# Optimization experiments

Hardware: AMD Instinct MI355X
Metric: run time of the kernel (lower is better)

Reference implementation:

```python
import jax, jax.numpy as jnp
import numpy as np

FACTOR = 5  # sampling factor c

def setup_inputs() -> dict:
    key = jax.random.key(0)
    k1, k2, k3, k4 = jax.random.split(key, 4)
    B, H, L, D = 4, 8, 2048, 64
    u = min(max(1, FACTOR * int(np.ceil(np.log(L)))), L)  # sample_k = 40
    return {
        "queries": jax.random.normal(k1, (B, H, L, D), jnp.float32),
        "keys": jax.random.normal(k2, (B, H, L, D), jnp.float32),
        "values": jax.random.normal(k3, (B, H, L, D), jnp.float32),
        "index_sample": jax.random.randint(k4, (L, u), 0, L, jnp.int32),
    }

def reference(queries, keys, values, index_sample):
    B, H, L_Q, D = queries.shape
    L_K = keys.shape[2]
    scale = 1.0 / np.sqrt(D)
    U_part = min(max(1, FACTOR * int(np.ceil(np.log(L_K)))), L_Q)  # n_top queries

    # --- _prob_QK: sampled scores + sparsity measure ---
    # K_sample[b,h,q,s,:] = keys[b,h,index_sample[q,s],:]  -> (B,H,L_Q,u,D)
    K_sample = keys[:, :, index_sample, :]
    QK_sample = jnp.einsum('bhqd,bhqsd->bhqs', queries, K_sample)  # (B,H,L_Q,u)
    M = QK_sample.max(-1) - QK_sample.sum(-1) / L_K                # (B,H,L_Q)
    _, index = jax.lax.top_k(M, U_part)                            # (B,H,U)

    # --- initial context: mean of V for non-selected queries ---
    context = jnp.broadcast_to(values.mean(-2, keepdims=True), (B, H, L_Q, D))

    # --- full attention for the top-U queries only ---
    Q_reduce = jnp.take_along_axis(queries, index[..., None], axis=2)   # (B,H,U,D)
    scores = jnp.einsum('bhud,bhkd->bhuk', Q_reduce, keys) * scale      # (B,H,U,L_K)
    attn = jax.nn.softmax(scores, axis=-1)
    out = jnp.einsum('bhuk,bhkd->bhud', attn, values)                   # (B,H,U,D)

    # --- scatter selected outputs back into the mean context ---
    bi = jnp.arange(B)[:, None, None]
    hi = jnp.arange(H)[None, :, None]
    context = context.at[bi, hi, index].set(out)
    return context
```

## Files before the change

### kernel.cpp

```cpp
#include <hip/hip_runtime.h>
#include <math.h>

#define Bq 4
#define Hh 8
#define Lh 2048
#define Dh 64
#define BH (Bq*Hh)

__global__ __launch_bounds__(256) void kAC(const float* __restrict__ Q,
                                           const float* __restrict__ K,
                                           const float* __restrict__ V,
                                           const int* __restrict__ idxs,
                                           float2* __restrict__ M2,
                                           float* __restrict__ vpart, int u) {
    int bi = blockIdx.x;
    int tid = threadIdx.x;
    if (bi >= 256) {
        int b2 = bi - 256;
        int xcd = b2 & 7, slot = b2 >> 3;
        int bh  = xcd * 4 + (slot >> 6);
        int q0  = (slot & 63) * 32;
        int lane = tid & 63, wv = tid >> 6;
        int g  = lane >> 4;
        int j  = lane & 15;
        int gb = lane & 48;
        int grp = wv * 4 + g;

        const float4* kb4 = (const float4*)(K + (long)bh * Lh * Dh);
        const float4* qb4 = (const float4*)(Q + (long)bh * Lh * Dh);

#define ROWS8(SOFF)                                                          \
        {                                                                    \
            float4 kf[8];                                                    \
            _Pragma("unroll")                                                \
            for (int r = 0; r < 8; ++r) {                                    \
                int idx = __shfl(ireg, gb + (SOFF) + r);                     \
                kf[r] = kb4[idx * 16 + j];                                   \
            }                                                                \
            _Pragma("unroll")                                                \
            for (int r = 0; r < 8; ++r) {                                    \
                float d = kf[r].x*qf.x + kf[r].y*qf.y                        \
                        + kf[r].z*qf.z + kf[r].w*qf.w;                       \
                d += __shfl_xor(d, 1);                                       \
                d += __shfl_xor(d, 2);                                       \
                d += __shfl_xor(d, 4);                                       \
                d += __shfl_xor(d, 8);                                       \
                mx = fmaxf(mx, d); sm += d;                                  \
            }                                                                \
        }

#pragma unroll 1
        for (int qq = 0; qq < 2; ++qq) {
            int q = q0 + grp * 2 + qq;
            float4 qf = qb4[q * 16 + j];
            const int* irow = idxs + (long)q * u;
            float mx = -INFINITY, sm = 0.f;

            int base = 0;
            int ireg = (j < u) ? irow[j] : 0;
            while (base + 16 <= u) {
                int iregN = (base + 16 + j < u) ? irow[base + 16 + j] : 0;
                ROWS8(0)
                ROWS8(8)
                ireg = iregN;
                base += 16;
            }
            int rem = u - base;
            int s = 0;
            if (rem >= 8) { ROWS8(0) s = 8; }
            for (; s < rem; ++s) {
                int idx = __shfl(ireg, gb + s);
                float4 kf0 = kb4[idx * 16 + j];
                float d = kf0.x*qf.x + kf0.y*qf.y + kf0.z*qf.z + kf0.w*qf.w;
                d += __shfl_xor(d, 1);
                d += __shfl_xor(d, 2);
                d += __shfl_xor(d, 4);
                d += __shfl_xor(d, 8);
                mx = fmaxf(mx, d); sm += d;
            }
            if (j == 0) M2[(long)bh * Lh + q] = make_float2(mx, sm);
        }
#undef ROWS8
    } else {
        int xcd = bi & 7, slot = bi >> 3;
        int bh = xcd * 4 + (slot >> 3);
        int chunk = slot & 7;
        int d = tid & 63, r0 = tid >> 6;
        const float* vb = V + ((long)bh * Lh + chunk * 256) * Dh;
        float s = 0.f;
        for (int i = 0; i < 64; ++i) s += vb[(r0 + 4 * i) * Dh + d];
        __shared__ float part[4][64];
        part[r0][d] = s;
        __syncthreads();
        if (tid < 64) {
            float t = part[0][tid] + part[1][tid] + part[2][tid] + part[3][tid];
            vpart[(bh * 8 + chunk) * 64 + tid] = t;
        }
    }
}

__global__ __launch_bounds__(256) void kBE(const float2* __restrict__ M2,
                                           const float* __restrict__ vpart,
                                           int* __restrict__ topk,
                                           float* __restrict__ ctx, int U) {
    int bi = blockIdx.x;
    int tid = threadIdx.x;
    if (bi >= 32) {
        long base = (long)(bi - 32) * 1024;
        int bh = (int)(base >> 17);
        __shared__ float vm[64];
        if (tid < 64) {
            float s = 0.f;
#pragma unroll
            for (int c2 = 0; c2 < 8; ++c2) s += vpart[(bh * 8 + c2) * 64 + tid];
            vm[tid] = s * (1.0f / (float)Lh);
        }
        __syncthreads();
        float4 val = *(const float4*)(vm + ((tid * 4) & 63));
        *(float4*)(ctx + base + tid * 4) = val;
        return;
    }
    int bh = bi;
    unsigned key[8];
#pragma unroll
    for (int j = 0; j < 8; ++j) {
        long q = (long)bh * Lh + tid + 256 * j;
        float2 mm = M2[q];
        float Mv = mm.x - mm.y * (1.0f / (float)Lh);
        unsigned ub = __float_as_uint(Mv);
        key[j] = ub ^ ((ub >> 31) ? 0xFFFFFFFFu : 0x80000000u);
    }
    __shared__ unsigned hist[256];
    __shared__ unsigned prefix_s;
    __shared__ int need_s;
    if (tid == 0) { prefix_s = 0u; need_s = U; }

    for (int level = 3; level >= 0; --level) {
        int shift = level * 8;
        hist[tid] = 0u;
        __syncthreads();
        unsigned prefix = prefix_s;
        int need = need_s;
        unsigned pmask = (level == 3) ? 0u : (0xFFFFFFFFu << (shift + 8));
#pragma unroll
        for (int j = 0; j < 8; ++j)
            if ((key[j] & pmask) == prefix)
                atomicAdd(&hist[(key[j] >> shift) & 0xFF], 1u);
        __syncthreads();
        if (tid < 64) {
            int lane = tid;
            unsigned h0 = hist[lane*4+0], h1 = hist[lane*4+1],
                     h2 = hist[lane*4+2], h3 = hist[lane*4+3];
            unsigned lt = h0 + h1 + h2 + h3;
            unsigned ssum = lt;
#pragma unroll
            for (int off = 1; off < 64; off <<= 1) {
                unsigned t = __shfl_down(ssum, off);
                if (lane + off < 64) ssum += t;
            }
            unsigned sx  = ssum - lt;
            unsigned suf3 = sx  + h3;
            unsigned suf2 = suf3 + h2;
            unsigned suf1 = suf2 + h1;
            unsigned suf0 = suf1 + h0;
            int localb = -1; unsigned nxt = 0u;
            if      ((int)suf3 >= need) { localb = lane*4+3; nxt = sx;   }
            else if ((int)suf2 >= need) { localb = lane*4+2; nxt = suf3; }
            else if ((int)suf1 >= need) { localb = lane*4+1; nxt = suf2; }
            else if ((int)suf0 >= need) { localb = lane*4+0; nxt = suf1; }
            unsigned long long ball = __ballot(localb >= 0);
            int hilane = 63 - __clzll(ball);
            if (lane == hilane) {
                prefix_s = prefix | ((unsigned)localb << shift);
                need_s = need - (int)nxt;
            }
        }
        __syncthreads();
    }
    unsigned T = prefix_s;
    int r = need_s;
    __shared__ int cgt, ceq;
    if (tid == 0) { cgt = 0; ceq = 0; }
    __syncthreads();
    int* out = topk + bh * U;
#pragma unroll
    for (int j = 0; j < 8; ++j) {
        if (key[j] > T) { int p = atomicAdd(&cgt, 1); out[p] = tid + 256 * j; }
        else if (key[j] == T) { int e = atomicAdd(&ceq, 1); if (e < r) out[U - r + e] = tid + 256 * j; }
    }
}

#define TK 64
__global__ __launch_bounds__(256) void kD_part(const float* __restrict__ Q,
                                               const float* __restrict__ K,
                                               const float* __restrict__ V,
                                               const int* __restrict__ topk,
                                               float* __restrict__ pm,
                                               float* __restrict__ pl,
                                               float* __restrict__ pacc,
                                               int U, int nch) {
    int bi = blockIdx.x;
    int xcd = bi & 7, slot = bi >> 3;
    int per = nch * 8;
    int bh = xcd * 4 + slot / per;
    int rest = slot % per;
    int uc = rest >> 3, kc = rest & 7;

    int tid = threadIdx.x;
    int wv = tid >> 6, lane = tid & 63;

    __shared__ float Qs[8 * 64];
    __shared__ float Ks[TK * 68];
    __shared__ float Ps[8 * 68];
    __shared__ float alph[8], mst[8], lst[8];
    __shared__ int   qidxs[8];
    float* accbuf = Ks;

    if (tid < 8) {
        int gu = uc * 8 + tid;
        qidxs[tid] = (gu < U) ? topk[bh * U + gu] : 0;
    }
    __syncthreads();
#pragma unroll
    for (int step = 0; step < 2; ++step) {
        int uu = step * 4 + wv;
        int row = qidxs[uu];
        Qs[uu * 64 + lane] = Q[((long)bh * Lh + row) * Dh + lane] * 0.125f;
    }

    int kq = lane, ug = wv;
    float mrun0 = -INFINITY, mrun1 = -INFINITY;
    float lrun0 = 0.f, lrun1 = 0.f;
    float accv[8] = {0.f,0.f,0.f,0.f,0.f,0.f,0.f,0.f};

    const long kvbase = (long)bh * Lh * Dh;
    const float4* Kg4 = (const float4*)(K + kvbase);
    const float*  Vg  = V + kvbase;
    int kbase0 = kc * 256;

    for (int t = 0; t < 4; ++t) {
        int t0 = kbase0 + t * TK;
        int f40 = t0 * (Dh / 4);
#pragma unroll
        for (int j = 0; j < 4; ++j) {
            int i = tid + 256 * j;
            float4 kv = Kg4[f40 + i];
            int row = i >> 4, col = i & 15;
            *(float4*)(&Ks[row * 68 + col * 4]) = kv;
        }
        __syncthreads();

        float s0 = 0.f, s1 = 0.f;
#pragma unroll
        for (int j16 = 0; j16 < 16; ++j16) {
            float4 kf = *(const float4*)(&Ks[kq * 68 + j16 * 4]);
            float4 qa = *(const float4*)(&Qs[(2 * ug + 0) * 64 + j16 * 4]);
            float4 qb = *(const float4*)(&Qs[(2 * ug + 1) * 64 + j16 * 4]);
            s0 += kf.x * qa.x + kf.y * qa.y + kf.z * qa.z + kf.w * qa.w;
            s1 += kf.x * qb.x + kf.y * qb.y + kf.z * qb.z + kf.w * qb.w;
        }
        float m0 = s0, m1 = s1;
#pragma unroll
        for (int off = 1; off < 64; off <<= 1) {
            m0 = fmaxf(m0, __shfl_xor(m0, off));
            m1 = fmaxf(m1, __shfl_xor(m1, off));
        }
        float mn0 = fmaxf(mrun0, m0), mn1 = fmaxf(mrun1, m1);
        float a0 = __expf(mrun0 - mn0), a1 = __expf(mrun1 - mn1);
        float p0 = __expf(s0 - mn0),  p1 = __expf(s1 - mn1);
        float ls0 = p0, ls1 = p1;
#pragma unroll
        for (int off = 1; off < 64; off <<= 1) {
            ls0 += __shfl_xor(ls0, off);
            ls1 += __shfl_xor(ls1, off);
        }
        lrun0 = a0 * lrun0 + ls0;  lrun1 = a1 * lrun1 + ls1;
        mrun0 = mn0;               mrun1 = mn1;
        Ps[(2 * ug + 0) * 68 + kq] = p0;
        Ps[(2 * ug + 1) * 68 + kq] = p1;
        if (lane == 0) { alph[2 * ug] = a0; alph[2 * ug + 1] = a1; }
        __syncthreads();

        float vk[16];
        int vrow0 = t0 + wv * 16;
#pragma unroll
        for (int k = 0; k < 16; ++k)
            vk[k] = Vg[(long)(vrow0 + k) * Dh + lane];
#pragma unroll
        for (int u2 = 0; u2 < 8; ++u2) {
            const float* pb = &Ps[u2 * 68 + wv * 16];
            float4 pA = *(const float4*)(pb + 0);
            float4 pB = *(const float4*)(pb + 4);
            float4 pC = *(const float4*)(pb + 8);
            float4 pD = *(const float4*)(pb + 12);
            float av = alph[u2];
            float ac = accv[u2] * av;
            ac += pA.x*vk[0]  + pA.y*vk[1]  + pA.z*vk[2]  + pA.w*vk[3];
            ac += pB.x*vk[4]  + pB.y*vk[5]  + pB.z*vk[6]  + pB.w*vk[7];
            ac += pC.x*vk[8]  + pC.y*vk[9]  + pC.z*vk[10] + pC.w*vk[11];
            ac += pD.x*vk[12] + pD.y*vk[13] + pD.z*vk[14] + pD.w*vk[15];
            accv[u2] = ac;
        }
    }

    if (lane == 0) {
        mst[2 * ug] = mrun0;     lst[2 * ug] = lrun0;
        mst[2 * ug + 1] = mrun1; lst[2 * ug + 1] = lrun1;
    }
#pragma unroll
    for (int u2 = 0; u2 < 8; ++u2)
        accbuf[wv * 512 + u2 * 64 + lane] = accv[u2];
    __syncthreads();

    int pbase = (bh * nch + uc) * 8;
    {
        int d = tid & 63, ua = tid >> 6;
#pragma unroll
        for (int h = 0; h < 2; ++h) {
            int u2 = ua + 4 * h;
            float o = accbuf[0 * 512 + u2 * 64 + d] + accbuf[1 * 512 + u2 * 64 + d]
                    + accbuf[2 * 512 + u2 * 64 + d] + accbuf[3 * 512 + u2 * 64 + d];
            pacc[((long)(pbase + u2) * 8 + kc) * 64 + d] = o;
        }
    }
    if (tid < 8) {
        int qp = (pbase + tid) * 8 + kc;
        pm[qp] = mst[tid];
        pl[qp] = lst[tid];
    }
}

__global__ __launch_bounds__(256) void kF_comb(const float* __restrict__ pm,
                                               const float* __restrict__ pl,
                                               const float* __restrict__ pacc,
                                               const int* __restrict__ topk,
                                               float* __restrict__ ctx,
                                               int U, int nch) {
    int bi = blockIdx.x;
    int bh = bi / nch, uc = bi % nch;
    int tid = threadIdx.x;
    int u = tid >> 5, t = tid & 31;
    int gu = uc * 8 + u;
    if (gu >= U) return;
    int qbase = (bh * nch + uc) * 8 + u;
    float m[8], l[8];
#pragma unroll
    for (int kc = 0; kc < 8; ++kc) { m[kc] = pm[qbase * 8 + kc]; l[kc] = pl[qbase * 8 + kc]; }
    float gm = m[0];
#pragma unroll
    for (int kc = 1; kc < 8; ++kc) gm = fmaxf(gm, m[kc]);
    float w[8]; float gl = 0.f;
#pragma unroll
    for (int kc = 0; kc < 8; ++kc) { w[kc] = __expf(m[kc] - gm); gl += l[kc] * w[kc]; }
    float inv = 1.0f / gl;
    float o0 = 0.f, o1 = 0.f;
#pragma unroll
    for (int kc = 0; kc < 8; ++kc) {
        const float* a = pacc + ((long)qbase * 8 + kc) * 64;
        o0 += a[t] * w[kc];
        o1 += a[t + 32] * w[kc];
    }
    int row = topk[bh * U + gu];
    float* crow = ctx + ((long)bh * Lh + row) * Dh;
    crow[t]      = o0 * inv;
    crow[t + 32] = o1 * inv;
}

extern "C" void kernel_launch(void* const* d_in, const int* in_sizes, int n_in,
                              void* d_out, int out_size, void* d_ws, size_t ws_size,
                              hipStream_t stream) {
    const float* Q    = (const float*)d_in[0];
    const float* K    = (const float*)d_in[1];
    const float* V    = (const float*)d_in[2];
    const int*   idxs = (const int*)d_in[3];
    float* ctx = (float*)d_out;

    int u = in_sizes[3] / Lh;
    int U = u;
    int nch = (U + 7) / 8;

    float*  wsf   = (float*)d_ws;
    float2* M2    = (float2*)wsf;
    int*    topk  = (int*)(wsf + 131072);
    float*  vpart = wsf + 131072 + 2048;
    float*  pm    = wsf + 149504;
    float*  pl    = pm + 32 * nch * 8 * 8;
    float*  pacc  = pl + 32 * nch * 8 * 8;

    kAC    <<<2304,         256, 0, stream>>>(Q, K, V, idxs, M2, vpart, u);
    kBE    <<<4128,         256, 0, stream>>>(M2, vpart, topk, ctx, U);
    kD_part<<<BH * nch * 8, 256, 0, stream>>>(Q, K, V, topk, pm, pl, pacc, U, nch);
    kF_comb<<<BH * nch,     256, 0, stream>>>(pm, pl, pacc, topk, ctx, U, nch);
}
```

Before: 159.9 us.

## Stage gathered key rows into LDS via async global_load_lds with swizzle

Rewrites the sampled-score part of the first kernel so each wave gathers the 40 sampled key rows per query straight into LDS using global_load_lds, with an XOR swizzle to avoid bank conflicts. The query rows are staged the same way, and the wave computes the dot products from LDS. Staged vmcnt waits let compute on earlier row groups overlap with loads still in flight, and the next query's indices are prefetched. A u==40 specialised path and a generic fallback are added, and LDS use rises to 48KB per block, which may lower occupancy.

```diff
diff --git a/kernel.cpp b/kernel.cpp
--- a/kernel.cpp
+++ b/kernel.cpp
@@ -6,6 +6,12 @@
 #define Lh 2048
 #define Dh 64
 #define BH (Bq*Hh)
+
+__device__ __forceinline__ void glds16(const void* g, void* l) {
+    __builtin_amdgcn_global_load_lds(
+        (const __attribute__((address_space(1))) void*)g,
+        (__attribute__((address_space(3))) void*)l, 16, 0, 0);
+}
 
 __global__ __launch_bounds__(256) void kAC(const float* __restrict__ Q,
                                            const float* __restrict__ K,
@@ -13,6 +19,7 @@
                                            const int* __restrict__ idxs,
                                            float2* __restrict__ M2,
                                            float* __restrict__ vpart, int u) {
+    __shared__ float lds[4 * 3072];
     int bi = blockIdx.x;
     int tid = threadIdx.x;
     if (bi >= 256) {
@@ -20,68 +27,137 @@
         int xcd = b2 & 7, slot = b2 >> 3;
         int bh  = xcd * 4 + (slot >> 6);
         int q0  = (slot & 63) * 32;
-        int lane = tid & 63, wv = tid >> 6;
-        int g  = lane >> 4;
-        int j  = lane & 15;
-        int gb = lane & 48;
-        int grp = wv * 4 + g;
-
-        const float4* kb4 = (const float4*)(K + (long)bh * Lh * Dh);
-        const float4* qb4 = (const float4*)(Q + (long)bh * Lh * Dh);
-
-#define ROWS8(SOFF)                                                          \
-        {                                                                    \
-            float4 kf[8];                                                    \
-            _Pragma("unroll")                                                \
-            for (int r = 0; r < 8; ++r) {                                    \
-                int idx = __shfl(ireg, gb + (SOFF) + r);                     \
-                kf[r] = kb4[idx * 16 + j];                                   \
-            }                                                                \
-            _Pragma("unroll")                                                \
-            for (int r = 0; r < 8; ++r) {                                    \
-                float d = kf[r].x*qf.x + kf[r].y*qf.y                        \
-                        + kf[r].z*qf.z + kf[r].w*qf.w;                       \
-                d += __shfl_xor(d, 1);                                       \
-                d += __shfl_xor(d, 2);                                       \
-                d += __shfl_xor(d, 4);                                       \
-                d += __shfl_xor(d, 8);                                       \
-                mx = fmaxf(mx, d); sm += d;                                  \
-            }                                                                \
-        }
-
+        int wv = tid >> 6, lane = tid & 63;
+        int hi = lane >> 4, lo = lane & 15;
+        int r7 = lo & 7;
+        float* wb  = lds + wv * 3072;
+        char*  wbc = (char*)wb;
+        const char* kcb = (const char*)(K + (long)bh * Lh * Dh);
+        long swzA = (long)((lo ^ hi) << 4);
+        long swzB = (long)((lo ^ hi ^ 4) << 4);
+        int ql0 = q0 + wv * 8;
+
+        {
+            const char* qgb = (const char*)(Q + ((long)bh * Lh + ql0) * Dh);
+            glds16(qgb + lane * 16, wbc + 10240);
+            glds16(qgb + 1024 + lane * 16, wbc + 10240 + 1024);
+        }
+
+        if (u == 40) {
+            int ireg = (lane < 40) ? idxs[(long)ql0 * 40 + lane] : 0;
 #pragma unroll 1
-        for (int qq = 0; qq < 2; ++qq) {
-            int q = q0 + grp * 2 + qq;
-            float4 qf = qb4[q * 16 + j];
-            const int* irow = idxs + (long)q * u;
-            float mx = -INFINITY, sm = 0.f;
-
-            int base = 0;
-            int ireg = (j < u) ? irow[j] : 0;
-            while (base + 16 <= u) {
-                int iregN = (base + 16 + j < u) ? irow[base + 16 + j] : 0;
-                ROWS8(0)
-                ROWS8(8)
+            for (int qi = 0; qi < 8; ++qi) {
+                int ql = ql0 + qi;
+#pragma unroll
+                for (int g = 0; g < 10; ++g) {
+                    int kidx = __shfl(ireg, 4 * g + hi);
+                    glds16(kcb + ((long)kidx << 8) + ((g & 1) ? swzB : swzA),
+                           wbc + g * 1024);
+                }
+                int qlN = (qi < 7) ? (ql + 1) : ql;
+                int iregN = (lane < 40) ? idxs[(long)qlN * 40 + lane] : 0;
+
+                const float* qrow = wb + 2560 + qi * 64;
+                float mx, sm;
+                asm volatile("s_waitcnt vmcnt(6)" ::: "memory");
+                __builtin_amdgcn_sched_barrier(0);
+                {
+                    float d = 0.f;
+#pragma unroll
+                    for (int j = 0; j < 4; ++j) {
+                        int s = 4 * j + hi, p = s ^ r7;
+                        float4 kf = *(const float4*)(wb + lo * 64 + p * 4);
+                        float4 qv = *(const float4*)(qrow + s * 4);
+                        d += kf.x*qv.x + kf.y*qv.y + kf.z*qv.z + kf.w*qv.w;
+                    }
+                    d += __shfl_xor(d, 16);
+                    d += __shfl_xor(d, 32);
+                    mx = d; sm = d;
+                }
+                asm volatile("s_waitcnt vmcnt(2)" ::: "memory");
+                __builtin_amdgcn_sched_barrier(0);
+                {
+                    float d = 0.f;
+#pragma unroll
+                    for (int j = 0; j < 4; ++j) {
+                        int s = 4 * j + hi, p = s ^ r7;
+                        float4 kf = *(const float4*)(wb + (16 + lo) * 64 + p * 4);
+                        float4 qv = *(const float4*)(qrow + s * 4);
+                        d += kf.x*qv.x + kf.y*qv.y + kf.z*qv.z + kf.w*qv.w;
+                    }
+                    d += __shfl_xor(d, 16);
+                    d += __shfl_xor(d, 32);
+                    mx = fmaxf(mx, d); sm += d;
+                }
+                asm volatile("s_waitcnt vmcnt(0)" ::: "memory");
+                __builtin_amdgcn_sched_barrier(0);
+                {
+                    float d = 0.f;
+#pragma unroll
+                    for (int j = 0; j < 4; ++j) {
+                        int s = 4 * j + hi, p = s ^ r7;
+                        float4 kf = *(const float4*)(wb + (32 + r7) * 64 + p * 4);
+                        float4 qv = *(const float4*)(qrow + s * 4);
+                        d += kf.x*qv.x + kf.y*qv.y + kf.z*qv.z + kf.w*qv.w;
+                    }
+                    d += __shfl_xor(d, 16);
+                    d += __shfl_xor(d, 32);
+                    if (lo < 8) { mx = fmaxf(mx, d); sm += d; }
+                }
+#pragma unroll
+                for (int off = 1; off < 16; off <<= 1) {
+                    mx = fmaxf(mx, __shfl_xor(mx, off));
+                    sm += __shfl_xor(sm, off);
+                }
+                if (lane == 0) M2[(long)bh * Lh + ql] = make_float2(mx, sm);
                 ireg = iregN;
-                base += 16;
             }
-            int rem = u - base;
-            int s = 0;
-            if (rem >= 8) { ROWS8(0) s = 8; }
-            for (; s < rem; ++s) {
-                int idx = __shfl(ireg, gb + s);
-                float4 kf0 = kb4[idx * 16 + j];
-                float d = kf0.x*qf.x + kf0.y*qf.y + kf0.z*qf.z + kf0.w*qf.w;
-                d += __shfl_xor(d, 1);
-                d += __shfl_xor(d, 2);
-                d += __shfl_xor(d, 4);
-                d += __shfl_xor(d, 8);
-                mx = fmaxf(mx, d); sm += d;
+        } else {
+#pragma unroll 1
+            for (int qi = 0; qi < 8; ++qi) {
+                int ql = ql0 + qi;
+                const float* qrow = wb + 2560 + qi * 64;
+                float mx = -INFINITY, sm = 0.f;
+                for (int cs = 0; cs < u; cs += 40) {
+                    int rows = u - cs; if (rows > 40) rows = 40;
+                    int ireg = idxs[(long)ql * u + cs + (lane < rows ? lane : 0)];
+                    int G = (rows + 3) >> 2;
+                    for (int g = 0; g < G; ++g) {
+                        int sl = 4 * g + hi; if (sl >= rows) sl = rows - 1;
+                        int kidx = __shfl(ireg, sl);
+                        glds16(kcb + ((long)kidx << 8) + ((g & 1) ? swzB : swzA),
+                               wbc + g * 1024);
+                    }
+                    asm volatile("s_waitcnt vmcnt(0)" ::: "memory");
+                    __builtin_amdgcn_sched_barrier(0);
+                    int NP = (rows + 15) >> 4;
+                    for (int P = 0; P < NP; ++P) {
+                        int row = 16 * P + lo;
+                        int rr = row < rows ? row : rows - 1;
+                        int rp = rr & 7;
+                        float d = 0.f;
+#pragma unroll
+                        for (int j = 0; j < 4; ++j) {
+                            int s = 4 * j + hi, p = s ^ rp;
+                            float4 kf = *(const float4*)(wb + rr * 64 + p * 4);
+                            float4 qv = *(const float4*)(qrow + s * 4);
+                            d += kf.x*qv.x + kf.y*qv.y + kf.z*qv.z + kf.w*qv.w;
+                        }
+                        d += __shfl_xor(d, 16);
+                        d += __shfl_xor(d, 32);
+                        if (row < rows) { mx = fmaxf(mx, d); sm += d; }
+                    }
+                }
+#pragma unroll
+                for (int off = 1; off < 16; off <<= 1) {
+                    mx = fmaxf(mx, __shfl_xor(mx, off));
+                    sm += __shfl_xor(sm, off);
+                }
+                if (lane == 0) M2[(long)bh * Lh + ql] = make_float2(mx, sm);
             }
-            if (j == 0) M2[(long)bh * Lh + q] = make_float2(mx, sm);
-        }
-#undef ROWS8
+        }
     } else {
+        float (*part)[64] = (float (*)[64])lds;
         int xcd = bi & 7, slot = bi >> 3;
         int bh = xcd * 4 + (slot >> 3);
         int chunk = slot & 7;
@@ -89,7 +165,6 @@
         const float* vb = V + ((long)bh * Lh + chunk * 256) * Dh;
         float s = 0.f;
         for (int i = 0; i < 64; ++i) s += vb[(r0 + 4 * i) * Dh + d];
-        __shared__ float part[4][64];
         part[r0][d] = s;
         __syncthreads();
         if (tid < 64) {
```

After: 174.7 us. +9.3%, slower.
